# Kernel optimization log

Hardware: AMD Instinct MI355X
Metric: run time of the kernel (lower is better)

Reference implementation:

```python
import jax, jax.numpy as jnp
import numpy as np


def setup_inputs() -> dict:
    key = jax.random.key(0)
    k1, k2 = jax.random.split(key)
    decoder_hidden = jax.random.normal(k1, (16, 1024, 1024), dtype=jnp.float32)
    encoder_outputs = jax.random.normal(k2, (16, 2048, 1024), dtype=jnp.float32)
    return {"decoder_hidden": decoder_hidden, "encoder_outputs": encoder_outputs}


def reference(decoder_hidden, encoder_outputs):
    # scores: [B, Q, K] = decoder_hidden @ encoder_outputs^T (no scaling, per source)
    scores = jnp.einsum('bqd,bkd->bqk', decoder_hidden, encoder_outputs)
    attn = jax.nn.softmax(scores, axis=-1)
    # context: [B, Q, D]
    context = jnp.einsum('bqk,bkd->bqd', attn, encoder_outputs)
    return (context, attn)
```

## Files before the change

### kernel.cpp

```cpp
#include <hip/hip_runtime.h>


typedef __attribute__((ext_vector_type(8))) short s8v;
typedef __attribute__((ext_vector_type(4))) float f32x4;
typedef __attribute__((ext_vector_type(8))) unsigned short us8;
typedef __attribute__((ext_vector_type(4))) unsigned short us4;

__device__ inline unsigned short f2bf(float f) {
    unsigned u = __builtin_bit_cast(unsigned, f);
    u += 0x7FFFu + ((u >> 16) & 1u);
    return (unsigned short)(u >> 16);
}
__device__ inline float bf2f(unsigned short h) {
    return __builtin_bit_cast(float, (unsigned)h << 16);
}

__global__ __launch_bounds__(256)
void split_convert(const float* __restrict__ x, unsigned short* __restrict__ hi,
                   unsigned short* __restrict__ lo, int n4)
{
    int i = blockIdx.x * 256 + threadIdx.x;
    const int stride = gridDim.x * 256;
    for (; i < n4; i += stride) {
        const float4 v = reinterpret_cast<const float4*>(x)[i];
        us4 h, l;
        h.x = f2bf(v.x); l.x = f2bf(v.x - bf2f(h.x));
        h.y = f2bf(v.y); l.y = f2bf(v.y - bf2f(h.y));
        h.z = f2bf(v.z); l.z = f2bf(v.z - bf2f(h.z));
        h.w = f2bf(v.w); l.w = f2bf(v.w - bf2f(h.w));
        reinterpret_cast<us4*>(hi)[i] = h;
        reinterpret_cast<us4*>(lo)[i] = l;
    }
}

__global__ __launch_bounds__(256)
void transpose_bf16(const unsigned short* __restrict__ in, unsigned short* __restrict__ out)
{
    __shared__ unsigned short S[64][72];
    const int b  = blockIdx.z;
    const int kt = blockIdx.x;
    const int dt = blockIdx.y;
    const unsigned short* ib = in  + (size_t)b * 2048 * 1024 + (size_t)kt * 64 * 1024 + (size_t)dt * 64;
    unsigned short*       ob = out + (size_t)b * 1024 * 2048 + (size_t)dt * 64 * 2048 + (size_t)kt * 64;

    const int tid = threadIdx.x;
    const int r0 = tid >> 3, c8 = (tid & 7) * 8;
    #pragma unroll
    for (int p = 0; p < 2; ++p) {
        const int r = r0 + 32 * p;
        const us8 v = *reinterpret_cast<const us8*>(&ib[(size_t)r * 1024 + c8]);
        *reinterpret_cast<us8*>(&S[r][c8]) = v;
    }
    __syncthreads();
    const int d0 = tid >> 3, k8 = (tid & 7) * 8;
    #pragma unroll
    for (int p = 0; p < 2; ++p) {
        const int d = d0 + 32 * p;
        us8 w;
        #pragma unroll
        for (int j = 0; j < 8; ++j) w[j] = S[k8 + j][d];
        *reinterpret_cast<us8*>(&ob[(size_t)d * 2048 + k8]) = w;
    }
}

template<int SPLIT>
__global__ __launch_bounds__(256, 2)
void gemm_nt_mfma(const unsigned short* __restrict__ Ah, const unsigned short* __restrict__ Al,
                  const unsigned short* __restrict__ Bh, const unsigned short* __restrict__ Bl,
                  float* __restrict__ Out, int ldA, int ldB, int ldO, int K,
                  long long sA, long long sB, long long sO)
{
    constexpr int NT = SPLIT ? 4 : 2;
    __shared__ unsigned short smem[NT * 4096];
    unsigned short* AsH = smem;
    unsigned short* BsH = smem + 4096;
    unsigned short* AsL = smem + (SPLIT ? 8192 : 0);
    unsigned short* BsL = smem + (SPLIT ? 12288 : 0);

    const int b = blockIdx.z, nt = blockIdx.x, mt = blockIdx.y;
    const int tid = threadIdx.x, lane = tid & 63, wid = tid >> 6;
    const int wm = wid >> 1, wn = wid & 1;

    const unsigned short* Ahb = Ah + b * sA + (size_t)(mt * 128) * ldA;
    const unsigned short* Bhb = Bh + b * sB + (size_t)(nt * 128) * ldB;
    const unsigned short* Alb = Al + b * sA + (size_t)(mt * 128) * ldA;
    const unsigned short* Blb = Bl + b * sB + (size_t)(nt * 128) * ldB;

    f32x4 acc[4][4];
    #pragma unroll
    for (int i = 0; i < 4; ++i)
        #pragma unroll
        for (int j = 0; j < 4; ++j) acc[i][j] = (f32x4){0.f, 0.f, 0.f, 0.f};

    const int l16 = lane * 16;
    auto stage = [&](unsigned short* tile, const unsigned short* src, int ld) {
        #pragma unroll
        for (int i = 0; i < 2; ++i) {
            const int o   = ((wid * 2 + i) << 10) + l16;
            const int row = o >> 6;
            const int ke  = (o & 63) >> 1;
            __builtin_amdgcn_global_load_lds(
                (const __attribute__((address_space(1))) void*)(src + (size_t)row * ld + ke),
                (__attribute__((address_space(3))) void*)(tile + ((wid * 2 + i) << 9)),
                16, 0, 0);
        }
    };

    const int fr = lane & 15;
    const int kg = (lane >> 4) << 3;

    for (int k0 = 0; k0 < K; k0 += 32) {
        stage(AsH, Ahb + k0, ldA);
        stage(BsH, Bhb + k0, ldB);
        if (SPLIT) { stage(AsL, Alb + k0, ldA); stage(BsL, Blb + k0, ldB); }
        __syncthreads();

        s8v ah[4], bh[4], al[4], bl[4];
        #pragma unroll
        for (int f = 0; f < 4; ++f) {
            ah[f] = *reinterpret_cast<const s8v*>(&AsH[(wm * 64 + f * 16 + fr) * 32 + kg]);
            bh[f] = *reinterpret_cast<const s8v*>(&BsH[(wn * 64 + f * 16 + fr) * 32 + kg]);
            if (SPLIT) {
                al[f] = *reinterpret_cast<const s8v*>(&AsL[(wm * 64 + f * 16 + fr) * 32 + kg]);
                bl[f] = *reinterpret_cast<const s8v*>(&BsL[(wn * 64 + f * 16 + fr) * 32 + kg]);
            }
        }
        #pragma unroll
        for (int fm = 0; fm < 4; ++fm)
            #pragma unroll
            for (int fn = 0; fn < 4; ++fn) {
                acc[fm][fn] = __builtin_amdgcn_mfma_f32_16x16x32_bf16(ah[fm], bh[fn], acc[fm][fn], 0, 0, 0);
                if (SPLIT) {
                    acc[fm][fn] = __builtin_amdgcn_mfma_f32_16x16x32_bf16(ah[fm], bl[fn], acc[fm][fn], 0, 0, 0);
                    acc[fm][fn] = __builtin_amdgcn_mfma_f32_16x16x32_bf16(al[fm], bh[fn], acc[fm][fn], 0, 0, 0);
                }
            }
        __syncthreads();
    }

    float* Ob = Out + b * sO + (size_t)(mt * 128 + wm * 64) * ldO + nt * 128 + wn * 64;
    const int cr = (lane >> 4) << 2;
    const int cc = lane & 15;
    #pragma unroll
    for (int fm = 0; fm < 4; ++fm)
        #pragma unroll
        for (int fn = 0; fn < 4; ++fn)
            #pragma unroll
            for (int r = 0; r < 4; ++r)
                Ob[(size_t)(fm * 16 + cr + r) * ldO + fn * 16 + cc] = acc[fm][fn][r];
}

__global__ __launch_bounds__(256)
void softmax_rows_bf(float* __restrict__ P, unsigned short* __restrict__ Pb)
{
    float* p = P + (size_t)blockIdx.x * 2048;
    unsigned short* pb = Pb + (size_t)blockIdx.x * 2048;
    const int tid = threadIdx.x;

    float4 v0 = *reinterpret_cast<const float4*>(&p[tid * 4]);
    float4 v1 = *reinterpret_cast<const float4*>(&p[1024 + tid * 4]);

    float m = fmaxf(fmaxf(fmaxf(v0.x, v0.y), fmaxf(v0.z, v0.w)),
                    fmaxf(fmaxf(v1.x, v1.y), fmaxf(v1.z, v1.w)));
    #pragma unroll
    for (int off = 32; off; off >>= 1) m = fmaxf(m, __shfl_xor(m, off));

    __shared__ float red[8];
    const int wid = tid >> 6;
    if ((tid & 63) == 0) red[wid] = m;
    __syncthreads();
    m = fmaxf(fmaxf(red[0], red[1]), fmaxf(red[2], red[3]));

    v0.x = __expf(v0.x - m); v0.y = __expf(v0.y - m);
    v0.z = __expf(v0.z - m); v0.w = __expf(v0.w - m);
    v1.x = __expf(v1.x - m); v1.y = __expf(v1.y - m);
    v1.z = __expf(v1.z - m); v1.w = __expf(v1.w - m);

    float s = ((v0.x + v0.y) + (v0.z + v0.w)) + ((v1.x + v1.y) + (v1.z + v1.w));
    #pragma unroll
    for (int off = 32; off; off >>= 1) s += __shfl_xor(s, off);
    if ((tid & 63) == 0) red[4 + wid] = s;
    __syncthreads();
    const float inv = 1.0f / ((red[4] + red[5]) + (red[6] + red[7]));

    v0.x *= inv; v0.y *= inv; v0.z *= inv; v0.w *= inv;
    v1.x *= inv; v1.y *= inv; v1.z *= inv; v1.w *= inv;
    *reinterpret_cast<float4*>(&p[tid * 4]) = v0;
    *reinterpret_cast<float4*>(&p[1024 + tid * 4]) = v1;

    us4 h0, h1;
    h0.x = f2bf(v0.x); h0.y = f2bf(v0.y); h0.z = f2bf(v0.z); h0.w = f2bf(v0.w);
    h1.x = f2bf(v1.x); h1.y = f2bf(v1.y); h1.z = f2bf(v1.z); h1.w = f2bf(v1.w);
    *reinterpret_cast<us4*>(&pb[tid * 4]) = h0;
    *reinterpret_cast<us4*>(&pb[1024 + tid * 4]) = h1;
}

#define BM 128
#define BN 128
#define BK 32
#define LDT 132

template <bool TRANSB>
__global__ __launch_bounds__(256, 2)
void gemm_tile(const float* __restrict__ X, const float* __restrict__ Y,
               float* __restrict__ Out,
               int ldX, int ldY, int ldO, int KD,
               long long strideX, long long strideY, long long strideO)
{
    __shared__ float As[BK][LDT];
    __shared__ float Bs[BK][LDT];
    const int b  = blockIdx.z;
    const int mt = blockIdx.y;
    const int nt = blockIdx.x;
    const float* Xb = X + (size_t)b * strideX + (size_t)mt * BM * ldX;
    const float* Yb = TRANSB ? (Y + (size_t)b * strideY + (size_t)nt * BN * ldY)
                             : (Y + (size_t)b * strideY + (size_t)nt * BN);
    float* Ob = Out + (size_t)b * strideO + (size_t)mt * BM * ldO + (size_t)nt * BN;
    const int tid = threadIdx.x;
    const int tx = tid & 15;
    const int ty = tid >> 4;
    const int sr = tid >> 3;
    const int sc = (tid & 7) << 2;
    const int br = tid >> 5;
    const int bc = (tid & 31) << 2;
    float acc[8][8];
    #pragma unroll
    for (int i = 0; i < 8; ++i)
        #pragma unroll
        for (int j = 0; j < 8; ++j) acc[i][j] = 0.f;
    for (int k0 = 0; k0 < KD; k0 += BK) {
        #pragma unroll
        for (int p = 0; p < 4; ++p) {
            const float4 v = *reinterpret_cast<const float4*>(
                &Xb[(size_t)(sr + 32 * p) * ldX + k0 + sc]);
            As[sc + 0][sr + 32 * p] = v.x;
            As[sc + 1][sr + 32 * p] = v.y;
            As[sc + 2][sr + 32 * p] = v.z;
            As[sc + 3][sr + 32 * p] = v.w;
        }
        if (TRANSB) {
            #pragma unroll
            for (int p = 0; p < 4; ++p) {
                const float4 v = *reinterpret_cast<const float4*>(
                    &Yb[(size_t)(sr + 32 * p) * ldY + k0 + sc]);
                Bs[sc + 0][sr + 32 * p] = v.x;
                Bs[sc + 1][sr + 32 * p] = v.y;
                Bs[sc + 2][sr + 32 * p] = v.z;
                Bs[sc + 3][sr + 32 * p] = v.w;
            }
        } else {
            #pragma unroll
            for (int p = 0; p < 4; ++p) {
                const float4 v = *reinterpret_cast<const float4*>(
                    &Yb[(size_t)(k0 + br + 8 * p) * ldY + bc]);
                *reinterpret_cast<float4*>(&Bs[br + 8 * p][bc]) = v;
            }
        }
        __syncthreads();
        #pragma unroll 8
        for (int kk = 0; kk < BK; ++kk) {
            const float4 a0 = *reinterpret_cast<const float4*>(&As[kk][ty * 4]);
            const float4 a1 = *reinterpret_cast<const float4*>(&As[kk][64 + ty * 4]);
            const float4 b0 = *reinterpret_cast<const float4*>(&Bs[kk][tx * 4]);
            const float4 b1 = *reinterpret_cast<const float4*>(&Bs[kk][64 + tx * 4]);
            const float av[8] = {a0.x, a0.y, a0.z, a0.w, a1.x, a1.y, a1.z, a1.w};
            const float bv[8] = {b0.x, b0.y, b0.z, b0.w, b1.x, b1.y, b1.z, b1.w};
            #pragma unroll
            for (int i = 0; i < 8; ++i)
                #pragma unroll
                for (int j = 0; j < 8; ++j)
                    acc[i][j] = fmaf(av[i], bv[j], acc[i][j]);
        }
        __syncthreads();
    }
    #pragma unroll
    for (int i = 0; i < 8; ++i) {
        const int r = (i < 4) ? (ty * 4 + i) : (64 + ty * 4 + (i - 4));
        const float4 w0 = make_float4(acc[i][0], acc[i][1], acc[i][2], acc[i][3]);
        const float4 w1 = make_float4(acc[i][4], acc[i][5], acc[i][6], acc[i][7]);
        *reinterpret_cast<float4*>(&Ob[(size_t)r * ldO + tx * 4])      = w0;
        *reinterpret_cast<float4*>(&Ob[(size_t)r * ldO + 64 + tx * 4]) = w1;
    }
}

__global__ __launch_bounds__(256)
void softmax_rows(float* __restrict__ P)
{
    float* p = P + (size_t)blockIdx.x * 2048;
    const int tid = threadIdx.x;
    float4 v0 = *reinterpret_cast<const float4*>(&p[tid * 4]);
    float4 v1 = *reinterpret_cast<const float4*>(&p[1024 + tid * 4]);
    float m = fmaxf(fmaxf(fmaxf(v0.x, v0.y), fmaxf(v0.z, v0.w)),
                    fmaxf(fmaxf(v1.x, v1.y), fmaxf(v1.z, v1.w)));
    #pragma unroll
    for (int off = 32; off; off >>= 1) m = fmaxf(m, __shfl_xor(m, off));
    __shared__ float red[8];
    const int wid = tid >> 6;
    if ((tid & 63) == 0) red[wid] = m;
    __syncthreads();
    m = fmaxf(fmaxf(red[0], red[1]), fmaxf(red[2], red[3]));
    v0.x = __expf(v0.x - m); v0.y = __expf(v0.y - m);
    v0.z = __expf(v0.z - m); v0.w = __expf(v0.w - m);
    v1.x = __expf(v1.x - m); v1.y = __expf(v1.y - m);
    v1.z = __expf(v1.z - m); v1.w = __expf(v1.w - m);
    float s = ((v0.x + v0.y) + (v0.z + v0.w)) + ((v1.x + v1.y) + (v1.z + v1.w));
    #pragma unroll
    for (int off = 32; off; off >>= 1) s += __shfl_xor(s, off);
    if ((tid & 63) == 0) red[4 + wid] = s;
    __syncthreads();
    const float inv = 1.0f / ((red[4] + red[5]) + (red[6] + red[7]));
    v0.x *= inv; v0.y *= inv; v0.z *= inv; v0.w *= inv;
    v1.x *= inv; v1.y *= inv; v1.z *= inv; v1.w *= inv;
    *reinterpret_cast<float4*>(&p[tid * 4]) = v0;
    *reinterpret_cast<float4*>(&p[1024 + tid * 4]) = v1;
}

extern "C" void kernel_launch(void* const* d_in, const int* in_sizes, int n_in,
                              void* d_out, int out_size, void* d_ws, size_t ws_size,
                              hipStream_t stream)
{
    const float* dec = (const float*)d_in[0];
    const float* enc = (const float*)d_in[1];
    float* ctx  = (float*)d_out;
    float* attn = ctx + (size_t)16 * 1024 * 1024;

    const long long DECN = 16LL * 1024 * 1024;
    const long long ENCN = 16LL * 2048 * 1024;
    const size_t NEED = (size_t)(2 * DECN + 4 * ENCN) * 2;

    if (ws_size >= NEED) {
        unsigned short* decH  = (unsigned short*)d_ws;
        unsigned short* decL  = decH + DECN;
        unsigned short* encH  = decL + DECN;
        unsigned short* encL  = encH + ENCN;
        unsigned short* encT  = encL + ENCN;
        unsigned short* attnB = encT + ENCN;

        split_convert<<<2048, 256, 0, stream>>>(dec, decH, decL, (int)(DECN / 4));
        split_convert<<<2048, 256, 0, stream>>>(enc, encH, encL, (int)(ENCN / 4));
        transpose_bf16<<<dim3(32, 16, 16), 256, 0, stream>>>(encH, encT);

        gemm_nt_mfma<1><<<dim3(16, 8, 16), 256, 0, stream>>>(
            decH, decL, encH, encL, attn,
            1024, 1024, 2048, 1024,
            1024LL * 1024, 2048LL * 1024, 1024LL * 2048);

        softmax_rows_bf<<<16 * 1024, 256, 0, stream>>>(attn, attnB);

        gemm_nt_mfma<0><<<dim3(8, 8, 16), 256, 0, stream>>>(
            attnB, attnB, encT, encT, ctx,
            2048, 2048, 1024, 2048,
            1024LL * 2048, 1024LL * 2048, 1024LL * 1024);
    } else {
        gemm_tile<true><<<dim3(2048 / BN, 1024 / BM, 16), 256, 0, stream>>>(
            dec, enc, attn, 1024, 1024, 2048, 1024,
            1024LL * 1024, 2048LL * 1024, 1024LL * 2048);
        softmax_rows<<<dim3(16 * 1024), 256, 0, stream>>>(attn);
        gemm_tile<false><<<dim3(1024 / BN, 1024 / BM, 16), 256, 0, stream>>>(
            attn, enc, ctx, 2048, 1024, 1024, 2048,
            1024LL * 2048, 2048LL * 1024, 1024LL * 1024);
    }
}
```

Measured before the change: 480.9 us.

## Replace bf16 MFMA GEMM with 256x256-tile, 4-stage pipelined, swizzled-LDS kernel

Replaces the 128x128 single-buffered MFMA GEMM with a 512-thread kernel that computes 256x256 output tiles. The three bf16-split products run as sequential K passes over one accumulator instead of three MFMAs per fragment. LDS loads are prefetched three stages ahead into a 4-deep ring with vmcnt-based waits, use an XOR swizzle to avoid bank conflicts, and the workgroup index is remapped for locality. This aims to raise arithmetic intensity and overlap global loads with MFMA work, at the cost of 128KB dynamic LDS and higher register pressure per block.

```diff
diff --git a/kernel.cpp b/kernel.cpp
--- a/kernel.cpp
+++ b/kernel.cpp
@@ -63,91 +63,129 @@
     }
 }
 
-template<int SPLIT>
-__global__ __launch_bounds__(256, 2)
-void gemm_nt_mfma(const unsigned short* __restrict__ Ah, const unsigned short* __restrict__ Al,
-                  const unsigned short* __restrict__ Bh, const unsigned short* __restrict__ Bl,
-                  float* __restrict__ Out, int ldA, int ldB, int ldO, int K,
-                  long long sA, long long sB, long long sO)
-{
-    constexpr int NT = SPLIT ? 4 : 2;
-    __shared__ unsigned short smem[NT * 4096];
-    unsigned short* AsH = smem;
-    unsigned short* BsH = smem + 4096;
-    unsigned short* AsL = smem + (SPLIT ? 8192 : 0);
-    unsigned short* BsL = smem + (SPLIT ? 12288 : 0);
-
-    const int b = blockIdx.z, nt = blockIdx.x, mt = blockIdx.y;
+template<int NPASS, int KPP, int NXT, int NYT>
+__global__ __launch_bounds__(512, 2)
+void gemm_nt_256(const unsigned short* __restrict__ A0,
+                 const unsigned short* __restrict__ A1,
+                 const unsigned short* __restrict__ A2,
+                 const unsigned short* __restrict__ B0,
+                 const unsigned short* __restrict__ B1,
+                 const unsigned short* __restrict__ B2,
+                 float* __restrict__ Out,
+                 const int ldA, const int ldB, const int ldO,
+                 const long long sA, const long long sB, const long long sO)
+{
+    constexpr int TPP = KPP / 32;
+    constexpr int NT  = NPASS * TPP;
+    extern __shared__ unsigned short smem[];
+
+    int flat = blockIdx.x + NXT * (blockIdx.y + NYT * (int)blockIdx.z);
+    const int nwg = NXT * NYT * (int)gridDim.z;
+    flat = (flat & 7) * (nwg >> 3) + (flat >> 3);
+    const int nt = flat % NXT;
+    const int mt = (flat / NXT) % NYT;
+    const int b  = flat / (NXT * NYT);
+
     const int tid = threadIdx.x, lane = tid & 63, wid = tid >> 6;
-    const int wm = wid >> 1, wn = wid & 1;
-
-    const unsigned short* Ahb = Ah + b * sA + (size_t)(mt * 128) * ldA;
-    const unsigned short* Bhb = Bh + b * sB + (size_t)(nt * 128) * ldB;
-    const unsigned short* Alb = Al + b * sA + (size_t)(mt * 128) * ldA;
-    const unsigned short* Blb = Bl + b * sB + (size_t)(nt * 128) * ldB;
-
-    f32x4 acc[4][4];
-    #pragma unroll
-    for (int i = 0; i < 4; ++i)
-        #pragma unroll
-        for (int j = 0; j < 4; ++j) acc[i][j] = (f32x4){0.f, 0.f, 0.f, 0.f};
-
-    const int l16 = lane * 16;
-    auto stage = [&](unsigned short* tile, const unsigned short* src, int ld) {
-        #pragma unroll
-        for (int i = 0; i < 2; ++i) {
-            const int o   = ((wid * 2 + i) << 10) + l16;
-            const int row = o >> 6;
-            const int ke  = (o & 63) >> 1;
-            __builtin_amdgcn_global_load_lds(
-                (const __attribute__((address_space(1))) void*)(src + (size_t)row * ld + ke),
-                (__attribute__((address_space(3))) void*)(tile + ((wid * 2 + i) << 9)),
-                16, 0, 0);
-        }
+    const int wm = wid >> 2, wn = wid & 3;
+
+    const size_t arow = (size_t)b * sA + (size_t)(mt * 256) * ldA;
+    const size_t brow = (size_t)b * sB + (size_t)(nt * 256) * ldB;
+    const unsigned short* Ap0 = A0 + arow;
+    const unsigned short* Ap1 = A1 + arow;
+    const unsigned short* Ap2 = A2 + arow;
+    const unsigned short* Bp0 = B0 + brow;
+    const unsigned short* Bp1 = B1 + brow;
+    const unsigned short* Bp2 = B2 + brow;
+
+    const int ci0 = tid, ci1 = 512 + tid;
+    const int r0 = ci0 >> 2, r1 = ci1 >> 2;
+    const int cs0 = ((ci0 & 3) ^ ((r0 >> 1) & 3)) * 8;
+    const int cs1 = ((ci1 & 3) ^ ((r1 >> 1) & 3)) * 8;
+    const int aoff0 = r0 * ldA + cs0, aoff1 = r1 * ldA + cs1;
+    const int boff0 = r0 * ldB + cs0, boff1 = r1 * ldB + cs1;
+    const int wd0 = wid * 512;
+    const int wd1 = 4096 + wid * 512;
+
+    auto stage = [&](int t) {
+        const int p  = t / TPP;
+        const int k0 = (t % TPP) * 32;
+        const unsigned short* As = (p == 0) ? Ap0 : (p == 1 ? Ap1 : Ap2);
+        const unsigned short* Bs = (p == 0) ? Bp0 : (p == 1 ? Bp1 : Bp2);
+        unsigned short* d = smem + (t & 3) * 16384;
+        __builtin_amdgcn_global_load_lds(
+            (const __attribute__((address_space(1))) void*)(As + k0 + aoff0),
+            (__attribute__((address_space(3))) void*)(d + wd0), 16, 0, 0);
+        __builtin_amdgcn_global_load_lds(
+            (const __attribute__((address_space(1))) void*)(As + k0 + aoff1),
+            (__attribute__((address_space(3))) void*)(d + wd1), 16, 0, 0);
+        __builtin_amdgcn_global_load_lds(
+            (const __attribute__((address_space(1))) void*)(Bs + k0 + boff0),
+            (__attribute__((address_space(3))) void*)(d + 8192 + wd0), 16, 0, 0);
+        __builtin_amdgcn_global_load_lds(
+            (const __attribute__((address_space(1))) void*)(Bs + k0 + boff1),
+            (__attribute__((address_space(3))) void*)(d + 8192 + wd1), 16, 0, 0);
     };
 
     const int fr = lane & 15;
-    const int kg = (lane >> 4) << 3;
-
-    for (int k0 = 0; k0 < K; k0 += 32) {
-        stage(AsH, Ahb + k0, ldA);
-        stage(BsH, Bhb + k0, ldB);
-        if (SPLIT) { stage(AsL, Alb + k0, ldA); stage(BsL, Blb + k0, ldB); }
-        __syncthreads();
-
-        s8v ah[4], bh[4], al[4], bl[4];
-        #pragma unroll
-        for (int f = 0; f < 4; ++f) {
-            ah[f] = *reinterpret_cast<const s8v*>(&AsH[(wm * 64 + f * 16 + fr) * 32 + kg]);
-            bh[f] = *reinterpret_cast<const s8v*>(&BsH[(wn * 64 + f * 16 + fr) * 32 + kg]);
-            if (SPLIT) {
-                al[f] = *reinterpret_cast<const s8v*>(&AsL[(wm * 64 + f * 16 + fr) * 32 + kg]);
-                bl[f] = *reinterpret_cast<const s8v*>(&BsL[(wn * 64 + f * 16 + fr) * 32 + kg]);
-            }
-        }
-        #pragma unroll
-        for (int fm = 0; fm < 4; ++fm)
+    const int kc = lane >> 4;
+    int offA[8], offB[4];
+    #pragma unroll
+    for (int m = 0; m < 8; ++m) {
+        const int R = wm * 128 + m * 16 + fr;
+        offA[m] = R * 32 + ((kc ^ ((R >> 1) & 3)) << 3);
+    }
+    #pragma unroll
+    for (int n = 0; n < 4; ++n) {
+        const int R = wn * 64 + n * 16 + fr;
+        offB[n] = 8192 + R * 32 + ((kc ^ ((R >> 1) & 3)) << 3);
+    }
+
+    f32x4 acc[8][4];
+    #pragma unroll
+    for (int m = 0; m < 8; ++m)
+        #pragma unroll
+        for (int n = 0; n < 4; ++n) acc[m][n] = (f32x4){0.f, 0.f, 0.f, 0.f};
+
+    stage(0); stage(1); stage(2);
+
+    for (int t = 0; t < NT; ++t) {
+        const int rem = NT - 1 - t;
+        if (rem >= 2)      asm volatile("s_waitcnt vmcnt(8)" ::: "memory");
+        else if (rem == 1) asm volatile("s_waitcnt vmcnt(4)" ::: "memory");
+        else               asm volatile("s_waitcnt vmcnt(0)" ::: "memory");
+        __builtin_amdgcn_s_barrier();
+        asm volatile("" ::: "memory");
+
+        const unsigned short* buf = smem + (t & 3) * 16384;
+        s8v bfrag[4], afrag[8];
+        #pragma unroll
+        for (int n = 0; n < 4; ++n) bfrag[n] = *reinterpret_cast<const s8v*>(buf + offB[n]);
+        #pragma unroll
+        for (int m = 0; m < 8; ++m) afrag[m] = *reinterpret_cast<const s8v*>(buf + offA[m]);
+
+        if (t + 3 < NT) stage(t + 3);
+
+        __builtin_amdgcn_s_setprio(1);
+        #pragma unroll
+        for (int m = 0; m < 8; ++m)
             #pragma unroll
-            for (int fn = 0; fn < 4; ++fn) {
-                acc[fm][fn] = __builtin_amdgcn_mfma_f32_16x16x32_bf16(ah[fm], bh[fn], acc[fm][fn], 0, 0, 0);
-                if (SPLIT) {
-                    acc[fm][fn] = __builtin_amdgcn_mfma_f32_16x16x32_bf16(ah[fm], bl[fn], acc[fm][fn], 0, 0, 0);
-                    acc[fm][fn] = __builtin_amdgcn_mfma_f32_16x16x32_bf16(al[fm], bh[fn], acc[fm][fn], 0, 0, 0);
-                }
-            }
-        __syncthreads();
-    }
-
-    float* Ob = Out + b * sO + (size_t)(mt * 128 + wm * 64) * ldO + nt * 128 + wn * 64;
+            for (int n = 0; n < 4; ++n)
+                acc[m][n] = __builtin_amdgcn_mfma_f32_16x16x32_bf16(afrag[m], bfrag[n], acc[m][n], 0, 0, 0);
+        __builtin_amdgcn_s_setprio(0);
+        asm volatile("" ::: "memory");
+    }
+
+    float* Ob = Out + (size_t)b * sO + (size_t)(mt * 256 + wm * 128) * ldO + nt * 256 + wn * 64;
     const int cr = (lane >> 4) << 2;
     const int cc = lane & 15;
     #pragma unroll
-    for (int fm = 0; fm < 4; ++fm)
-        #pragma unroll
-        for (int fn = 0; fn < 4; ++fn)
+    for (int m = 0; m < 8; ++m)
+        #pragma unroll
+        for (int n = 0; n < 4; ++n)
             #pragma unroll
             for (int r = 0; r < 4; ++r)
-                Ob[(size_t)(fm * 16 + cr + r) * ldO + fn * 16 + cc] = acc[fm][fn][r];
+                Ob[(size_t)(m * 16 + cr + r) * ldO + n * 16 + cc] = acc[m][n][r];
 }
 
 __global__ __launch_bounds__(256)
@@ -302,7 +340,7 @@
     v0.x = __expf(v0.x - m); v0.y = __expf(v0.y - m);
     v0.z = __expf(v0.z - m); v0.w = __expf(v0.w - m);
     v1.x = __expf(v1.x - m); v1.y = __expf(v1.y - m);
-    v1.z = __expf(v1.z - m); v1.w = __expf(v1.w - m);
+    v1.w = __expf(v1.w - m); v1.z = __expf(v1.z - m);
     float s = ((v0.x + v0.y) + (v0.z + v0.w)) + ((v1.x + v1.y) + (v1.z + v1.w));
     #pragma unroll
     for (int off = 32; off; off >>= 1) s += __shfl_xor(s, off);
@@ -336,20 +374,25 @@
         unsigned short* encT  = encL + ENCN;
         unsigned short* attnB = encT + ENCN;
 
+        hipFuncSetAttribute((const void*)&gemm_nt_256<3, 1024, 8, 4>,
+                            hipFuncAttributeMaxDynamicSharedMemorySize, 131072);
+        hipFuncSetAttribute((const void*)&gemm_nt_256<1, 2048, 4, 4>,
+                            hipFuncAttributeMaxDynamicSharedMemorySize, 131072);
+
         split_convert<<<2048, 256, 0, stream>>>(dec, decH, decL, (int)(DECN / 4));
         split_convert<<<2048, 256, 0, stream>>>(enc, encH, encL, (int)(ENCN / 4));
         transpose_bf16<<<dim3(32, 16, 16), 256, 0, stream>>>(encH, encT);
 
-        gemm_nt_mfma<1><<<dim3(16, 8, 16), 256, 0, stream>>>(
-            decH, decL, encH, encL, attn,
-            1024, 1024, 2048, 1024,
+        gemm_nt_256<3, 1024, 8, 4><<<dim3(8, 4, 16), 512, 131072, stream>>>(
+            decH, decH, decL, encH, encL, encH, attn,
+            1024, 1024, 2048,
             1024LL * 1024, 2048LL * 1024, 1024LL * 2048);
 
         softmax_rows_bf<<<16 * 1024, 256, 0, stream>>>(attn, attnB);
 
-        gemm_nt_mfma<0><<<dim3(8, 8, 16), 256, 0, stream>>>(
-            attnB, attnB, encT, encT, ctx,
-            2048, 2048, 1024, 2048,
+        gemm_nt_256<1, 2048, 4, 4><<<dim3(4, 4, 16), 512, 131072, stream>>>(
+            attnB, attnB, attnB, encT, encT, encT, ctx,
+            2048, 2048, 1024,
             1024LL * 2048, 1024LL * 2048, 1024LL * 1024);
     } else {
         gemm_tile<true><<<dim3(2048 / BN, 1024 / BM, 16), 256, 0, stream>>>(
```

Result: slower. 530.0 us (+10.2%).
